# Kernel tuning notes

Hardware: AMD Instinct MI355X
Metric: run time of the kernel (lower is better)

Reference implementation:

```python
import jax, jax.numpy as jnp
import numpy as np

B, L, K, NR, S = 512, 1024, 8, 512, 20  # batch, seq_len, n_matrices, n_rates, alphabet
EXT = 26  # extended alphabet (20 std aa + 6 special), pad of 6 in call()


def _expm(A):
    """Differentiable matrix exponential for small batched matrices (..., n, n).
    Scaling-and-squaring with an order-16 Taylor series (fixed 6 squarings).
    Matches tf.linalg.expm to high accuracy for the small-norm tau*Q here."""
    SQ = 6
    A = A / jnp.asarray(2.0 ** SQ, A.dtype)
    n = A.shape[-1]
    I = jnp.eye(n, dtype=A.dtype)
    P = I + A
    T = A
    for i in range(2, 17):
        T = jnp.matmul(T, A) / i
        P = P + T
    for _ in range(SQ):
        P = jnp.matmul(P, P)
    return P


def setup_inputs() -> dict:
    key = jax.random.key(0)
    k1, k2, k3, k4, k5 = jax.random.split(key, 5)
    return {
        "inputs": jax.random.randint(k1, (B, L), 0, EXT, dtype=jnp.int32),
        "rate_indices": jax.random.randint(k2, (B,), 0, NR, dtype=jnp.int32),
        "tau_kernel": jax.random.normal(k3, (NR,), dtype=jnp.float32),
        "exchangeability_kernel": jax.random.normal(k4, (K, S, S), dtype=jnp.float32),
        "frequencies": jax.random.uniform(k5, (S,), dtype=jnp.float32, minval=0.01, maxval=1.0),
    }


def reference(inputs, rate_indices, tau_kernel, exchangeability_kernel, frequencies):
    b, l = inputs.shape
    mask = inputs < S                                   # (b, L) std-aa mask
    std = jnp.where(mask, inputs, 0)                    # clamp special tokens to 0
    maskf = mask.astype(jnp.float32)[:, :, None, None]  # (b, L, 1, 1)

    # make_R: symmetrize, softplus, zero diagonal
    eye = jnp.eye(S, dtype=jnp.float32)
    R = jax.nn.softplus(0.5 * (exchangeability_kernel + jnp.swapaxes(exchangeability_kernel, -1, -2)))
    R = R * (1.0 - eye)

    # make_rate_matrix: Q = R * pi, subtract row-sum diagonal, normalize by expected rate
    Q = R * frequencies[None, None, :]                  # (k, s, s)
    diag = jnp.sum(Q, axis=-1, keepdims=True)           # (k, s, 1)
    Q = Q - diag * eye
    mue = jnp.sum(frequencies[None, :, None] * diag, axis=-2, keepdims=True)  # (k, 1, 1)
    Q = Q / jnp.maximum(mue, 1e-16)

    # per-sequence evolutionary times
    tau = jax.nn.softplus(tau_kernel)[rate_indices]     # (b,)

    # batched small-matrix expm: (b, k, s, s)
    P = _expm(tau[:, None, None, None] * Q[None])

    # gather ancestral probability rows: (b, L, k, s)
    anc = P[jnp.arange(b)[:, None], :, std, :]
    anc = anc * maskf
    anc = jnp.pad(anc, ((0, 0), (0, 0), (0, 0), (0, EXT - S)))  # pad 20 -> 26
    rest = jax.nn.one_hot(inputs, EXT, dtype=jnp.float32)[:, :, None, :] * (1.0 - maskf)
    anc = anc + rest                                    # (b, L, k, 26)
    return anc.reshape(b, l, -1)                        # (b, L, k*26)
```

## Files before the change

### kernel.cpp

```cpp
#include <hip/hip_runtime.h>
#include <math.h>

#define B   512
#define L   1024
#define K   8
#define NR  512
#define S   20
#define EXT 26
#define SS  (S*S)
#define ROWF (K*EXT)
#define BROW (L*ROWF)
#define HROW (BROW/2)

__device__ __forceinline__ float softplusf(float x) {
    return fmaxf(x, 0.0f) + log1pf(expf(-fabsf(x)));
}

__global__ __launch_bounds__(256) void expm_kernel(
    const float* __restrict__ exch,
    const float* __restrict__ freq,
    const float* __restrict__ tau_kernel,
    const int*   __restrict__ rate_indices,
    float* __restrict__ out)
{
    int blk = blockIdx.x;
    int b = blk / K, kk = blk % K;

    __shared__ float Ash[SS];
    __shared__ float Tbuf[2][SS];
    __shared__ float diag_sh[S];
    __shared__ float mue_sh;
    __shared__ float tau_sh;

    int t = threadIdx.x;

    const float* E = exch + kk * SS;
    for (int e = t; e < SS; e += 256) {
        int r = e / S, c = e % S;
        float v = 0.f;
        if (r != c) {
            float x = 0.5f * (E[r*S + c] + E[c*S + r]);
            v = softplusf(x) * freq[c];
        }
        Tbuf[0][e] = v;
    }
    if (t == 0) tau_sh = softplusf(tau_kernel[rate_indices[b]]);
    __syncthreads();

    if (t < S) {
        float d = 0.f;
        #pragma unroll
        for (int j = 0; j < S; ++j) d += Tbuf[0][t*S + j];
        diag_sh[t] = d;
    }
    __syncthreads();

    if (t == 0) {
        float m = 0.f;
        #pragma unroll
        for (int s = 0; s < S; ++s) m += freq[s] * diag_sh[s];
        mue_sh = fmaxf(m, 1e-16f);
    }
    __syncthreads();

    float scale = tau_sh * 0.015625f;
    for (int e = t; e < SS; e += 256) {
        int r = e / S, c = e % S;
        float v = (r == c) ? -diag_sh[r] : Tbuf[0][e];
        Ash[e] = (v / mue_sh) * scale;
    }
    __syncthreads();

    int e0 = t;
    int e1 = t + 256;
    int r0 = e0 / S, c0 = e0 % S;
    bool has1 = (e1 < SS);
    int r1 = has1 ? (e1 / S) : 0, c1 = has1 ? (e1 % S) : 0;

    float acol0[S], acol1[S];
    #pragma unroll
    for (int j = 0; j < S; ++j) {
        acol0[j] = Ash[j*S + c0];
        acol1[j] = has1 ? Ash[j*S + c1] : 0.f;
    }

    float p0 = Ash[e0] + ((r0 == c0) ? 1.f : 0.f);
    float p1 = has1 ? (Ash[e1] + ((r1 == c1) ? 1.f : 0.f)) : 0.f;

    const float* Tcur = Ash;
    int cur = 0;
    for (int i = 2; i <= 16; ++i) {
        float inv = 1.0f / (float)i;
        float t0 = 0.f, t1 = 0.f;
        const float* Trow0 = Tcur + r0 * S;
        const float* Trow1 = Tcur + r1 * S;
        #pragma unroll
        for (int j = 0; j < S; ++j) {
            t0 += Trow0[j] * acol0[j];
            t1 += Trow1[j] * acol1[j];
        }
        t0 *= inv; t1 *= inv;
        Tbuf[cur][e0] = t0;
        if (has1) Tbuf[cur][e1] = t1;
        p0 += t0; p1 += t1;
        __syncthreads();
        Tcur = Tbuf[cur];
        cur ^= 1;
    }

    for (int sq = 0; sq < 6; ++sq) {
        Tbuf[cur][e0] = p0;
        if (has1) Tbuf[cur][e1] = p1;
        __syncthreads();
        const float* Pb = Tbuf[cur];
        float n0 = 0.f, n1 = 0.f;
        #pragma unroll
        for (int j = 0; j < S; ++j) {
            n0 += Pb[r0*S + j] * Pb[j*S + c0];
            n1 += Pb[r1*S + j] * Pb[j*S + c1];
        }
        p0 = n0; p1 = n1;
        cur ^= 1;
    }

    size_t obase = (size_t)b * BROW + (size_t)kk * SS;
    out[obase + e0] = p0;
    out[obase + HROW + e0] = p0;
    if (has1) {
        out[obase + e1] = p1;
        out[obase + HROW + e1] = p1;
    }
}

__global__ __launch_bounds__(512, 8) void write_kernel(
    const int* __restrict__ inputs,
    float* __restrict__ out)
{
    __shared__ __align__(16) float Psh[K*SS];
    __shared__ __align__(16) float Row[EXT*ROWF];
    __shared__ int inp_sh[512];

    int blk = blockIdx.x;
    int b = blk >> 1, h = blk & 1;
    int t = threadIdx.x;

    float* base = out + (size_t)b * BROW + (size_t)h * HROW;

    const float4* src4 = (const float4*)base;
    float4* Psh4 = (float4*)Psh;
    for (int u = t; u < (K*SS)/4; u += 512) Psh4[u] = src4[u];
    inp_sh[t] = inputs[b * L + h * (L/2) + t];
    __syncthreads();

    for (int u = t; u < EXT*ROWF; u += 512) {
        int row = u / ROWF;
        int c   = u - row * ROWF;
        int k   = c / EXT;
        int s   = c - k * EXT;
        float v;
        if (row < S) v = (s < S) ? Psh[k*SS + row*S + s] : 0.f;
        else         v = (s == row) ? 1.f : 0.f;
        Row[u] = v;
    }
    __syncthreads();

    float4* out4 = (float4*)base;
    for (int u = t; u < (L/2) * (ROWF/4); u += 512) {
        int l = u / (ROWF/4);
        int q = u - l * (ROWF/4);
        const float4* r4 = (const float4*)(Row + inp_sh[l] * ROWF);
        out4[u] = r4[q];
    }
}

extern "C" void kernel_launch(void* const* d_in, const int* in_sizes, int n_in,
                              void* d_out, int out_size, void* d_ws, size_t ws_size,
                              hipStream_t stream) {
    const int*   inputs  = (const int*)  d_in[0];
    const int*   rate_ix = (const int*)  d_in[1];
    const float* tau_k   = (const float*)d_in[2];
    const float* exch    = (const float*)d_in[3];
    const float* freq    = (const float*)d_in[4];
    float* out = (float*)d_out;

    (void)d_ws; (void)ws_size;

    expm_kernel<<<B * K, 256, 0, stream>>>(exch, freq, tau_k, rate_ix, out);
    write_kernel<<<B * 2, 512, 0, stream>>>(inputs, out);
}
```

Baseline: 511.2 us.

## Register-tile expm matmuls 3x3 per thread with single-wavefront blocks

Rewrites the expm kernel to use 64-thread blocks, where each thread computes a 3x3 register tile of the 20x20 (padded to 24x24) matrix products. Rows are read with float4 LDS loads, so A and T values are reused across the tile. This cuts LDS traffic and instruction count per FMA and removes idle threads from the old 256-thread layout. In exchange it adds padding overhead and per-thread register pressure, and gives less parallelism per block.

```diff
diff --git a/kernel.cpp b/kernel.cpp
--- a/kernel.cpp
+++ b/kernel.cpp
@@ -8,6 +8,7 @@
 #define S   20
 #define EXT 26
 #define SS  (S*S)
+#define PD  24
 #define ROWF (K*EXT)
 #define BROW (L*ROWF)
 #define HROW (BROW/2)
@@ -16,7 +17,7 @@
     return fmaxf(x, 0.0f) + log1pf(expf(-fabsf(x)));
 }
 
-__global__ __launch_bounds__(256) void expm_kernel(
+__global__ __launch_bounds__(64, 4) void expm_kernel(
     const float* __restrict__ exch,
     const float* __restrict__ freq,
     const float* __restrict__ tau_kernel,
@@ -26,35 +27,35 @@
     int blk = blockIdx.x;
     int b = blk / K, kk = blk % K;
 
-    __shared__ float Ash[SS];
-    __shared__ float Tbuf[2][SS];
+    __shared__ __align__(16) float M0[PD*PD];
+    __shared__ __align__(16) float M1[PD*PD];
     __shared__ float diag_sh[S];
-    __shared__ float mue_sh;
-    __shared__ float tau_sh;
+    __shared__ float mue_sh, tau_sh;
 
     int t = threadIdx.x;
+    int li = t >> 3, lj = t & 7;
+    int r0 = 3*li, c0 = 3*lj;
+
+    for (int e = t; e < PD*PD; e += 64) { M0[e] = 0.f; M1[e] = 0.f; }
+    if (t == 0) tau_sh = softplusf(tau_kernel[rate_indices[b]]);
+    __syncthreads();
 
     const float* E = exch + kk * SS;
-    for (int e = t; e < SS; e += 256) {
-        int r = e / S, c = e % S;
+    for (int e = t; e < SS; e += 64) {
+        int r = e / S, c = e - r*S;
         float v = 0.f;
-        if (r != c) {
-            float x = 0.5f * (E[r*S + c] + E[c*S + r]);
-            v = softplusf(x) * freq[c];
-        }
-        Tbuf[0][e] = v;
-    }
-    if (t == 0) tau_sh = softplusf(tau_kernel[rate_indices[b]]);
-    __syncthreads();
-
+        if (r != c)
+            v = softplusf(0.5f * (E[r*S + c] + E[c*S + r])) * freq[c];
+        M0[r*PD + c] = v;
+    }
+    __syncthreads();
     if (t < S) {
         float d = 0.f;
         #pragma unroll
-        for (int j = 0; j < S; ++j) d += Tbuf[0][t*S + j];
+        for (int j = 0; j < S; ++j) d += M0[t*PD + j];
         diag_sh[t] = d;
     }
     __syncthreads();
-
     if (t == 0) {
         float m = 0.f;
         #pragma unroll
@@ -64,71 +65,119 @@
     __syncthreads();
 
     float scale = tau_sh * 0.015625f;
-    for (int e = t; e < SS; e += 256) {
-        int r = e / S, c = e % S;
-        float v = (r == c) ? -diag_sh[r] : Tbuf[0][e];
-        Ash[e] = (v / mue_sh) * scale;
-    }
-    __syncthreads();
-
-    int e0 = t;
-    int e1 = t + 256;
-    int r0 = e0 / S, c0 = e0 % S;
-    bool has1 = (e1 < SS);
-    int r1 = has1 ? (e1 / S) : 0, c1 = has1 ? (e1 % S) : 0;
-
-    float acol0[S], acol1[S];
+    for (int e = t; e < SS; e += 64) {
+        int r = e / S, c = e - r*S;
+        float v = (r == c) ? -diag_sh[r] : M0[r*PD + c];
+        M0[r*PD + c] = (v / mue_sh) * scale;
+    }
+    __syncthreads();
+
+    float Ac[S][3];
     #pragma unroll
     for (int j = 0; j < S; ++j) {
-        acol0[j] = Ash[j*S + c0];
-        acol1[j] = has1 ? Ash[j*S + c1] : 0.f;
-    }
-
-    float p0 = Ash[e0] + ((r0 == c0) ? 1.f : 0.f);
-    float p1 = has1 ? (Ash[e1] + ((r1 == c1) ? 1.f : 0.f)) : 0.f;
-
-    const float* Tcur = Ash;
-    int cur = 0;
+        #pragma unroll
+        for (int d = 0; d < 3; ++d)
+            Ac[j][d] = M0[j*PD + c0 + d];
+    }
+
+    float P[3][3];
+    #pragma unroll
+    for (int dr = 0; dr < 3; ++dr)
+        #pragma unroll
+        for (int dc = 0; dc < 3; ++dc) {
+            int r = r0 + dr, c = c0 + dc;
+            P[dr][dc] = M0[r*PD + c] + ((r == c && r < S) ? 1.f : 0.f);
+        }
+
+    const float* Tc = M0;
+    float* Tn = M1;
+    #pragma unroll 1
     for (int i = 2; i <= 16; ++i) {
+        float C[3][3] = {{0.f,0.f,0.f},{0.f,0.f,0.f},{0.f,0.f,0.f}};
+        #pragma unroll
+        for (int jc = 0; jc < 5; ++jc) {
+            float4 a0 = *(const float4*)&Tc[(r0+0)*PD + 4*jc];
+            float4 a1 = *(const float4*)&Tc[(r0+1)*PD + 4*jc];
+            float4 a2 = *(const float4*)&Tc[(r0+2)*PD + 4*jc];
+            float t0[4] = {a0.x, a0.y, a0.z, a0.w};
+            float t1[4] = {a1.x, a1.y, a1.z, a1.w};
+            float t2[4] = {a2.x, a2.y, a2.z, a2.w};
+            #pragma unroll
+            for (int dj = 0; dj < 4; ++dj) {
+                int j = 4*jc + dj;
+                #pragma unroll
+                for (int dc = 0; dc < 3; ++dc) {
+                    C[0][dc] = fmaf(t0[dj], Ac[j][dc], C[0][dc]);
+                    C[1][dc] = fmaf(t1[dj], Ac[j][dc], C[1][dc]);
+                    C[2][dc] = fmaf(t2[dj], Ac[j][dc], C[2][dc]);
+                }
+            }
+        }
         float inv = 1.0f / (float)i;
-        float t0 = 0.f, t1 = 0.f;
-        const float* Trow0 = Tcur + r0 * S;
-        const float* Trow1 = Tcur + r1 * S;
-        #pragma unroll
-        for (int j = 0; j < S; ++j) {
-            t0 += Trow0[j] * acol0[j];
-            t1 += Trow1[j] * acol1[j];
-        }
-        t0 *= inv; t1 *= inv;
-        Tbuf[cur][e0] = t0;
-        if (has1) Tbuf[cur][e1] = t1;
-        p0 += t0; p1 += t1;
+        #pragma unroll
+        for (int dr = 0; dr < 3; ++dr)
+            #pragma unroll
+            for (int dc = 0; dc < 3; ++dc) {
+                C[dr][dc] *= inv;
+                P[dr][dc] += C[dr][dc];
+                Tn[(r0+dr)*PD + c0 + dc] = C[dr][dc];
+            }
         __syncthreads();
-        Tcur = Tbuf[cur];
-        cur ^= 1;
-    }
-
+        float* tmp = (float*)Tc; Tc = Tn; Tn = tmp;
+    }
+
+    #pragma unroll 1
     for (int sq = 0; sq < 6; ++sq) {
-        Tbuf[cur][e0] = p0;
-        if (has1) Tbuf[cur][e1] = p1;
+        #pragma unroll
+        for (int dr = 0; dr < 3; ++dr)
+            #pragma unroll
+            for (int dc = 0; dc < 3; ++dc)
+                Tn[(r0+dr)*PD + c0 + dc] = P[dr][dc];
         __syncthreads();
-        const float* Pb = Tbuf[cur];
-        float n0 = 0.f, n1 = 0.f;
-        #pragma unroll
-        for (int j = 0; j < S; ++j) {
-            n0 += Pb[r0*S + j] * Pb[j*S + c0];
-            n1 += Pb[r1*S + j] * Pb[j*S + c1];
-        }
-        p0 = n0; p1 = n1;
-        cur ^= 1;
+        const float* Pb = Tn;
+        float C[3][3] = {{0.f,0.f,0.f},{0.f,0.f,0.f},{0.f,0.f,0.f}};
+        #pragma unroll
+        for (int jc = 0; jc < 5; ++jc) {
+            float4 a0 = *(const float4*)&Pb[(r0+0)*PD + 4*jc];
+            float4 a1 = *(const float4*)&Pb[(r0+1)*PD + 4*jc];
+            float4 a2 = *(const float4*)&Pb[(r0+2)*PD + 4*jc];
+            float t0[4] = {a0.x, a0.y, a0.z, a0.w};
+            float t1[4] = {a1.x, a1.y, a1.z, a1.w};
+            float t2[4] = {a2.x, a2.y, a2.z, a2.w};
+            float cb[4][3];
+            #pragma unroll
+            for (int dj = 0; dj < 4; ++dj)
+                #pragma unroll
+                for (int dc = 0; dc < 3; ++dc)
+                    cb[dj][dc] = Pb[(4*jc + dj)*PD + c0 + dc];
+            #pragma unroll
+            for (int dj = 0; dj < 4; ++dj)
+                #pragma unroll
+                for (int dc = 0; dc < 3; ++dc) {
+                    C[0][dc] = fmaf(t0[dj], cb[dj][dc], C[0][dc]);
+                    C[1][dc] = fmaf(t1[dj], cb[dj][dc], C[1][dc]);
+                    C[2][dc] = fmaf(t2[dj], cb[dj][dc], C[2][dc]);
+                }
+        }
+        #pragma unroll
+        for (int dr = 0; dr < 3; ++dr)
+            #pragma unroll
+            for (int dc = 0; dc < 3; ++dc)
+                P[dr][dc] = C[dr][dc];
+        float* tmp = (float*)Tc; Tc = Tn; Tn = tmp;
     }
 
     size_t obase = (size_t)b * BROW + (size_t)kk * SS;
-    out[obase + e0] = p0;
-    out[obase + HROW + e0] = p0;
-    if (has1) {
-        out[obase + e1] = p1;
-        out[obase + HROW + e1] = p1;
+    #pragma unroll
+    for (int dr = 0; dr < 3; ++dr) {
+        int r = r0 + dr; if (r >= S) continue;
+        #pragma unroll
+        for (int dc = 0; dc < 3; ++dc) {
+            int c = c0 + dc; if (c >= S) continue;
+            float v = P[dr][dc];
+            out[obase + r*S + c] = v;
+            out[obase + HROW + r*S + c] = v;
+        }
     }
 }
 
@@ -185,6 +234,6 @@
 
     (void)d_ws; (void)ws_size;
 
-    expm_kernel<<<B * K, 256, 0, stream>>>(exch, freq, tau_k, rate_ix, out);
+    expm_kernel<<<B * K, 64, 0, stream>>>(exch, freq, tau_k, rate_ix, out);
     write_kernel<<<B * 2, 512, 0, stream>>>(inputs, out);
 }
```

Result: no change. 504.2 us (-1.4%).
